# Performance work log

Hardware: AMD Instinct MI355X
Metric: run time of the kernel (lower is better)

The kernel has to match this reference:

```python
import jax, jax.numpy as jnp
import numpy as np

N_NODES = 100000
N_EDGES = 500000
E_HID = 64
IN_DIM = 192  # r_hidden + 2*t_hidden
NEG_SLOPE = 0.01


def setup_inputs() -> dict:
    key = jax.random.key(0)
    ks = jax.random.split(key, 16)
    s_in = 1.0 / np.sqrt(IN_DIM)
    s_e = 1.0 / np.sqrt(E_HID)
    inp = {
        "x_e": jax.random.normal(ks[0], (N_NODES, E_HID), dtype=jnp.float32),
        "x_r": jax.random.normal(ks[1], (N_EDGES, IN_DIM), dtype=jnp.float32),
        "edge_index": jax.random.randint(ks[2], (2, N_EDGES), 0, N_NODES, dtype=jnp.int64),
        "rel_size": jnp.arange(N_EDGES, dtype=jnp.int64),
        "Wr": jax.random.uniform(ks[3], (E_HID, IN_DIM), jnp.float32, -s_in, s_in),
        "br": jax.random.uniform(ks[4], (E_HID,), jnp.float32, -s_in, s_in),
        "Wr1": jax.random.uniform(ks[5], (E_HID, IN_DIM), jnp.float32, -s_in, s_in),
        "br1": jax.random.uniform(ks[6], (E_HID,), jnp.float32, -s_in, s_in),
        "Wr2": jax.random.uniform(ks[7], (E_HID, IN_DIM), jnp.float32, -s_in, s_in),
        "br2": jax.random.uniform(ks[8], (E_HID,), jnp.float32, -s_in, s_in),
        "ah": jax.random.uniform(ks[9], (E_HID,), jnp.float32, -s_e, s_e),
        "ah1": jax.random.uniform(ks[10], (E_HID,), jnp.float32, -s_e, s_e),
        "at": jax.random.uniform(ks[11], (E_HID,), jnp.float32, -s_e, s_e),
        "ar1": jax.random.uniform(ks[12], (E_HID,), jnp.float32, -s_e, s_e),
        "ar2": jax.random.uniform(ks[13], (E_HID,), jnp.float32, -s_e, s_e),
        "ar3": jax.random.uniform(ks[14], (E_HID,), jnp.float32, -s_e, s_e),
    }
    return inp


def _gat_block(x_e, x_r, idx, rel_size, W, b, a_node, a_rel, num_nodes):
    # e_r = w_r(x_r): [E, e_hid]
    e_r = x_r @ W.T + b
    # attention logits per edge: a_node . x_e[idx] + a_rel . e_r
    logits = x_e[idx] @ a_node + e_r @ a_rel  # [E]
    lr = jnp.where(logits > 0, logits, NEG_SLOPE * logits)  # leaky_relu
    # segment softmax over destination segments (idx)
    m = jax.ops.segment_max(lr, idx, num_segments=num_nodes)
    ex = jnp.exp(lr - m[idx])
    s = jax.ops.segment_sum(ex, idx, num_segments=num_nodes)
    alpha = ex / (s[idx] + 1e-16)
    # spmm: out[n] = sum_{e: idx[e]==n} alpha[e] * e_r[rel_size[e]]
    agg = jax.ops.segment_sum(alpha[:, None] * e_r[rel_size], idx, num_segments=num_nodes)
    return x_e + jax.nn.relu(agg)


def reference(x_e, x_r, edge_index, rel_size, Wr, br, Wr1, br1, Wr2, br2,
              ah, ah1, at, ar1, ar2, ar3):
    n = x_e.shape[0]
    h, t = edge_index[0], edge_index[1]
    x_e = _gat_block(x_e, x_r, h, rel_size, Wr, br, ah, ar1, n)
    x_e = _gat_block(x_e, x_r, t, rel_size, Wr1, br1, at, ar2, n)
    x_e = _gat_block(x_e, x_r, h, rel_size, Wr2, br2, ah1, ar3, n)
    return x_e
```

## Files before the change

kernel.cpp:

```cpp
#include <hip/hip_runtime.h>
#include <hip/hip_bf16.h>

typedef __attribute__((ext_vector_type(8))) short short8;
typedef __attribute__((ext_vector_type(4))) float f32x4;

#define DEV __device__ __forceinline__

#define BARRIER() do { asm volatile("s_waitcnt lgkmcnt(0)" ::: "memory"); \
                       __builtin_amdgcn_s_barrier(); \
                       __builtin_amdgcn_sched_barrier(0); } while (0)

DEV unsigned short f2bf(float f) {
    unsigned u = __float_as_uint(f);
    u += 0x7FFFu + ((u >> 16) & 1u);
    return (unsigned short)(u >> 16);
}
DEV float bf2f(unsigned short h) { return __uint_as_float(((unsigned)h) << 16); }
DEV unsigned pk2(float lo, float hi) {
    float2 f; f.x = lo; f.y = hi;
    __hip_bfloat162 h = __float22bfloat162_rn(f);
    unsigned r; __builtin_memcpy(&r, &h, 4);
    return r;
}
union S8 { short8 s; unsigned u[4]; };

__global__ __launch_bounds__(256) void wconv_k(
    const float* __restrict__ W0, const float* __restrict__ W1,
    const float* __restrict__ W2, unsigned short* __restrict__ wbf)
{
    const int i = blockIdx.x * 256 + threadIdx.x;
    if (i >= 3 * 64 * 192) return;
    const int m = i / (64 * 192), r = i % (64 * 192);
    const float* W = (m == 0) ? W0 : ((m == 1) ? W1 : W2);
    wbf[i] = f2bf(W[r]);
}

__global__ __launch_bounds__(256) void gemm_k(
    const float* __restrict__ xr, const unsigned short* __restrict__ wbf,
    const float* __restrict__ b0, const float* __restrict__ b1, const float* __restrict__ b2,
    const float* __restrict__ a0, const float* __restrict__ a1, const float* __restrict__ a2,
    unsigned short* __restrict__ er,
    float* __restrict__ ed0, float* __restrict__ ed1, float* __restrict__ ed2,
    int E, int ntiles, int K)
{
    __shared__ unsigned short As[64 * 192];
    __shared__ float red[12][64];
    const int t = threadIdx.x;
    const int w = t >> 6, l = t & 63, l15 = l & 15, lg = l >> 4;
    const int srow = t >> 2, sq = t & 3;

    short8 bfr[3][6];
#pragma unroll
    for (int i = 0; i < 3; ++i) {
        const int gc = (w * 3 + i) * 16 + l15;
#pragma unroll
        for (int ks = 0; ks < 6; ++ks)
            bfr[i][ks] = *(const short8*)&wbf[(size_t)gc * 192 + ks * 32 + lg * 8];
    }
    float4 biasf[3], arf[3];
#pragma unroll
    for (int i = 0; i < 3; ++i) {
        const int ct = w * 3 + i, m = ct >> 2;
        const int cb_ = ((ct & 3) << 4) + (lg << 2);
        const float* bp = (m == 0) ? b0 : ((m == 1) ? b1 : b2);
        const float* ap = (m == 0) ? a0 : ((m == 1) ? a1 : a2);
        biasf[i] = *(const float4*)(bp + cb_);
        arf[i]  = *(const float4*)(ap + cb_);
    }

    const int G = gridDim.x;
    float4 nv[12];
    if (blockIdx.x < ntiles) {
        const long e = (long)blockIdx.x * 64 + srow;
        const bool ok = e < E;
        const float* sp = xr + e * (long)K + sq * 48;
#pragma unroll
        for (int r = 0; r < 3; ++r)
#pragma unroll
            for (int g2 = 0; g2 < 4; ++g2)
                nv[r * 4 + g2] = ok ? *(const float4*)(sp + r * 16 + g2 * 4)
                                    : make_float4(0.f, 0.f, 0.f, 0.f);
    }

    for (int tile = blockIdx.x; tile < ntiles; tile += G) {
        const long e0 = (long)tile * 64;
        BARRIER();
        {
            const unsigned swz = (unsigned)((srow & 7) << 4);
#pragma unroll
            for (int r = 0; r < 3; ++r) {
                S8 o0, o1;
                o0.u[0] = pk2(nv[r * 4 + 0].x, nv[r * 4 + 0].y);
                o0.u[1] = pk2(nv[r * 4 + 0].z, nv[r * 4 + 0].w);
                o0.u[2] = pk2(nv[r * 4 + 1].x, nv[r * 4 + 1].y);
                o0.u[3] = pk2(nv[r * 4 + 1].z, nv[r * 4 + 1].w);
                o1.u[0] = pk2(nv[r * 4 + 2].x, nv[r * 4 + 2].y);
                o1.u[1] = pk2(nv[r * 4 + 2].z, nv[r * 4 + 2].w);
                o1.u[2] = pk2(nv[r * 4 + 3].x, nv[r * 4 + 3].y);
                o1.u[3] = pk2(nv[r * 4 + 3].z, nv[r * 4 + 3].w);
                const unsigned byte0 = (unsigned)(srow * 384 + (sq * 48 + r * 16) * 2);
                *(short8*)((char*)As + (byte0 ^ swz)) = o0.s;
                *(short8*)((char*)As + ((byte0 + 16) ^ swz)) = o1.s;
            }
        }
        {
            const int nxt = tile + G;
            if (nxt < ntiles) {
                const long e = (long)nxt * 64 + srow;
                const bool ok = e < E;
                const float* sp = xr + e * (long)K + sq * 48;
#pragma unroll
                for (int r = 0; r < 3; ++r)
#pragma unroll
                    for (int g2 = 0; g2 < 4; ++g2)
                        nv[r * 4 + g2] = ok ? *(const float4*)(sp + r * 16 + g2 * 4)
                                            : make_float4(0.f, 0.f, 0.f, 0.f);
            }
        }
        BARRIER();
        f32x4 acc[4][3];
#pragma unroll
        for (int rt = 0; rt < 4; ++rt)
#pragma unroll
            for (int i = 0; i < 3; ++i) acc[rt][i] = (f32x4)(0.f);
#pragma unroll
        for (int ks = 0; ks < 6; ++ks) {
            short8 af[4];
#pragma unroll
            for (int rt = 0; rt < 4; ++rt) {
                const int row = rt * 16 + l15;
                const unsigned byte = (unsigned)(row * 384 + ks * 64 + lg * 16);
                af[rt] = *(const short8*)((const char*)As + (byte ^ ((row & 7) << 4)));
            }
#pragma unroll
            for (int i = 0; i < 3; ++i)
#pragma unroll
                for (int rt = 0; rt < 4; ++rt)
                    acc[rt][i] = __builtin_amdgcn_mfma_f32_16x16x32_bf16(bfr[i][ks], af[rt], acc[rt][i], 0, 0, 0);
        }
#pragma unroll
        for (int i = 0; i < 3; ++i) {
            const int fb = (w * 3 + i) * 16 + (lg << 2);
#pragma unroll
            for (int rt = 0; rt < 4; ++rt) {
                const int edge = rt * 16 + l15;
                const long ee = e0 + edge;
                const float v0 = acc[rt][i][0] + biasf[i].x;
                const float v1 = acc[rt][i][1] + biasf[i].y;
                const float v2 = acc[rt][i][2] + biasf[i].z;
                const float v3 = acc[rt][i][3] + biasf[i].w;
                if (ee < E) {
                    uint2 pkv;
                    pkv.x = pk2(v0, v1);
                    pkv.y = pk2(v2, v3);
                    *(uint2*)(er + (size_t)ee * 192 + fb) = pkv;
                }
                float pd = v0 * arf[i].x + v1 * arf[i].y + v2 * arf[i].z + v3 * arf[i].w;
                pd += __shfl_xor(pd, 16);
                pd += __shfl_xor(pd, 32);
                if (lg == 0) red[w * 3 + i][edge] = pd;
            }
        }
        BARRIER();
        if (t < 64) {
            const long ee = e0 + t;
            if (ee < E) {
                float s0 = 0.f, s1 = 0.f, s2 = 0.f;
#pragma unroll
                for (int q = 0; q < 4; ++q) {
                    s0 += red[q][t]; s1 += red[4 + q][t]; s2 += red[8 + q][t];
                }
                ed0[ee] = s0; ed1[ee] = s1; ed2[ee] = s2;
            }
        }
    }
}

__global__ __launch_bounds__(256) void count2_k(const int* __restrict__ h,
                                                const int* __restrict__ tt,
                                                int* __restrict__ deg, int E, int N)
{
    const int e = blockIdx.x * 256 + threadIdx.x;
    if (e >= E) return;
    atomicAdd(&deg[h[e]], 1);
    atomicAdd(&deg[N + tt[e]], 1);
}

__global__ __launch_bounds__(256) void scan1_k(const int* __restrict__ deg,
                                               int* __restrict__ incl,
                                               int* __restrict__ bsum, int M)
{
    __shared__ int buf[256];
    const int tid = threadIdx.x;
    const int n = blockIdx.x * 256 + tid;
    buf[tid] = (n < M) ? deg[n] : 0;
    __syncthreads();
    for (int d = 1; d < 256; d <<= 1) {
        int v = (tid >= d) ? buf[tid - d] : 0;
        __syncthreads();
        buf[tid] += v;
        __syncthreads();
    }
    if (n < M) incl[n] = buf[tid];
    if (tid == 255) bsum[blockIdx.x] = buf[255];
}

__global__ __launch_bounds__(256) void scan2_k(int* __restrict__ bsum, int nb)
{
    __shared__ int wsum[4];
    const int tid = threadIdx.x, l = tid & 63, wv = tid >> 6;
    int base = 0;
    for (int start = 0; start < nb; start += 1024) {
        const int i0 = start + tid * 4;
        int v0 = 0, v1 = 0, v2 = 0, v3 = 0;
        if (i0 < nb)     v0 = bsum[i0];
        if (i0 + 1 < nb) v1 = bsum[i0 + 1];
        if (i0 + 2 < nb) v2 = bsum[i0 + 2];
        if (i0 + 3 < nb) v3 = bsum[i0 + 3];
        const int tsum = v0 + v1 + v2 + v3;
        int sc = tsum;
#pragma unroll
        for (int d = 1; d < 64; d <<= 1) {
            const int o = __shfl_up(sc, d);
            if (l >= d) sc += o;
        }
        if (l == 63) wsum[wv] = sc;
        __syncthreads();
        int woff = base;
        for (int q = 0; q < wv; ++q) woff += wsum[q];
        int run = woff + sc - tsum;
        run += v0; if (i0 < nb)     bsum[i0] = run;
        run += v1; if (i0 + 1 < nb) bsum[i0 + 1] = run;
        run += v2; if (i0 + 2 < nb) bsum[i0 + 2] = run;
        run += v3; if (i0 + 3 < nb) bsum[i0 + 3] = run;
        base += wsum[0] + wsum[1] + wsum[2] + wsum[3];
        __syncthreads();
    }
}

__global__ __launch_bounds__(256) void off_k(const int* __restrict__ deg,
                                             const int* __restrict__ incl,
                                             const int* __restrict__ bsum,
                                             int* __restrict__ off,
                                             int* __restrict__ cur, int M, int tot)
{
    const int n = blockIdx.x * 256 + threadIdx.x;
    if (n < M) {
        const int prev = (blockIdx.x > 0) ? bsum[blockIdx.x - 1] : 0;
        const int o = prev + incl[n] - deg[n];
        off[n] = o;
        cur[n] = o;
    }
    if (n == 0) off[M] = tot;
}

__global__ __launch_bounds__(256) void fill2_k(const int* __restrict__ h,
                                               const int* __restrict__ tt,
                                               int* __restrict__ cur,
                                               int* __restrict__ elist, int E, int N)
{
    const int e = blockIdx.x * 256 + threadIdx.x;
    if (e >= E) return;
    const int p = atomicAdd(&cur[h[e]], 1);
    elist[p] = e;
    const int p2 = atomicAdd(&cur[N + tt[e]], 1);
    elist[p2] = e;
}

__global__ __launch_bounds__(256, 4) void gat3_k(
    const int* __restrict__ off, const int* __restrict__ elist,
    const float* __restrict__ ed0, const float* __restrict__ ed1,
    const float* __restrict__ ed2, const unsigned short* __restrict__ er,
    const float* __restrict__ xe, float* __restrict__ out,
    const float* __restrict__ an0, const float* __restrict__ an1,
    const float* __restrict__ an2, int N)
{
    __shared__ float sm[4][8][64];
    const int wv = threadIdx.x >> 6;
    const int node = blockIdx.x * 4 + wv;
    if (node >= N) return;
    const int l = threadIdx.x & 63;
    const int g = l >> 3, q = l & 7;

    float x = xe[(size_t)node * 64 + l];

#pragma unroll
    for (int b = 0; b < 3; ++b) {
        const float* edb = (b == 0) ? ed0 : ((b == 1) ? ed1 : ed2);
        const float* anb = (b == 0) ? an0 : ((b == 1) ? an1 : an2);
        const int* offb = off + ((b == 1) ? N : 0);
        const int cb = b * 64;
        const int s0 = offb[node], s1 = offb[node + 1];

        float pv = x * anb[l];
#pragma unroll
        for (int d = 1; d < 64; d <<= 1) pv += __shfl_xor(pv, d);

        float m = -1e30f, s = 0.f;
        f32x4 aA = (f32x4)(0.f), aB = (f32x4)(0.f);
        for (int j = s0; j < s1; j += 8) {
            const int jj = j + g;
            if (jj < s1) {
                const int e = elist[jj];
                const float lg_ = pv + edb[e];
                const float lv = lg_ > 0.f ? lg_ : 0.01f * lg_;
                const short8 v = *(const short8*)(er + (size_t)e * 192 + cb + q * 8);
                const float nm = fmaxf(m, lv);
                const float rs = __expf(m - nm);
                const float wg = __expf(lv - nm);
                s = s * rs + wg;
                aA[0] = aA[0] * rs + wg * bf2f((unsigned short)v[0]);
                aA[1] = aA[1] * rs + wg * bf2f((unsigned short)v[1]);
                aA[2] = aA[2] * rs + wg * bf2f((unsigned short)v[2]);
                aA[3] = aA[3] * rs + wg * bf2f((unsigned short)v[3]);
                aB[0] = aB[0] * rs + wg * bf2f((unsigned short)v[4]);
                aB[1] = aB[1] * rs + wg * bf2f((unsigned short)v[5]);
                aB[2] = aB[2] * rs + wg * bf2f((unsigned short)v[6]);
                aB[3] = aB[3] * rs + wg * bf2f((unsigned short)v[7]);
                m = nm;
            }
        }
        float mt = m;
        mt = fmaxf(mt, __shfl_xor(mt, 8));
        mt = fmaxf(mt, __shfl_xor(mt, 16));
        mt = fmaxf(mt, __shfl_xor(mt, 32));
        const float rs2 = __expf(m - mt);
        s *= rs2;
        s += __shfl_xor(s, 8);
        s += __shfl_xor(s, 16);
        s += __shfl_xor(s, 32);
#pragma unroll
        for (int c = 0; c < 4; ++c) { aA[c] *= rs2; aB[c] *= rs2; }
        *(f32x4*)&sm[wv][g][q * 8] = aA;
        *(f32x4*)&sm[wv][g][q * 8 + 4] = aB;
        asm volatile("s_waitcnt lgkmcnt(0)" ::: "memory");
        __builtin_amdgcn_sched_barrier(0);
        float a = 0.f;
#pragma unroll
        for (int gg = 0; gg < 8; ++gg) a += sm[wv][gg][l];
        asm volatile("s_waitcnt lgkmcnt(0)" ::: "memory");
        __builtin_amdgcn_sched_barrier(0);

        x += fmaxf(a / (s + 1e-16f), 0.f);
    }
    out[(size_t)node * 64 + l] = x;
}

extern "C" void kernel_launch(void* const* d_in, const int* in_sizes, int n_in,
                              void* d_out, int out_size, void* d_ws, size_t ws_size,
                              hipStream_t stream)
{
    const float* xe  = (const float*)d_in[0];
    const float* xr  = (const float*)d_in[1];
    const int*   eix = (const int*)d_in[2];
    const float* Wr  = (const float*)d_in[4];
    const float* br  = (const float*)d_in[5];
    const float* Wr1 = (const float*)d_in[6];
    const float* br1 = (const float*)d_in[7];
    const float* Wr2 = (const float*)d_in[8];
    const float* br2 = (const float*)d_in[9];
    const float* ah  = (const float*)d_in[10];
    const float* ah1 = (const float*)d_in[11];
    const float* at_ = (const float*)d_in[12];
    const float* ar1 = (const float*)d_in[13];
    const float* ar2 = (const float*)d_in[14];
    const float* ar3 = (const float*)d_in[15];

    const int E = in_sizes[3];
    const int N = in_sizes[0] / 64;
    const int K = in_sizes[1] / E;
    const int M = 2 * N;
    float* out = (float*)d_out;

    char* p = (char*)d_ws;
    auto carve = [&](size_t bytes) -> void* {
        void* r = (void*)p;
        p += (bytes + 255) & ~(size_t)255;
        return r;
    };
    const int nb = (M + 255) / 256;
    unsigned short* er = (unsigned short*)carve((size_t)(E + 64) * 192 * 2);
    float* ed0 = (float*)carve((size_t)(E + 64) * 4);
    float* ed1 = (float*)carve((size_t)(E + 64) * 4);
    float* ed2 = (float*)carve((size_t)(E + 64) * 4);
    unsigned short* wbf = (unsigned short*)carve((size_t)3 * 64 * 192 * 2);
    int* off = (int*)carve((size_t)(M + 1) * 4);
    int* elist = (int*)carve((size_t)2 * E * 4);
    int* deg = (int*)carve((size_t)M * 4);
    int* incl = (int*)carve((size_t)M * 4);
    int* cur = (int*)carve((size_t)M * 4);
    int* bsum = (int*)carve((size_t)nb * 4);
    (void)ws_size;

    const int Eg = (E + 255) / 256;
    const int ng = (N + 3) / 4;
    const int ntiles = (E + 63) / 64;
    const int ggrid = ntiles < 1536 ? ntiles : 1536;

    wconv_k<<<(3 * 64 * 192 + 255) / 256, 256, 0, stream>>>(Wr, Wr1, Wr2, wbf);

    hipMemsetAsync(deg, 0, (size_t)M * 4, stream);
    count2_k<<<Eg, 256, 0, stream>>>(eix, eix + E, deg, E, N);
    scan1_k<<<nb, 256, 0, stream>>>(deg, incl, bsum, M);
    scan2_k<<<1, 256, 0, stream>>>(bsum, nb);
    off_k<<<nb, 256, 0, stream>>>(deg, incl, bsum, off, cur, M, 2 * E);
    fill2_k<<<Eg, 256, 0, stream>>>(eix, eix + E, cur, elist, E, N);

    gemm_k<<<ggrid, 256, 0, stream>>>(xr, wbf, br, br1, br2, ar1, ar2, ar3,
                                      er, ed0, ed1, ed2, E, ntiles, K);

    gat3_k<<<ng, 256, 0, stream>>>(off, elist, ed0, ed1, ed2, er, xe, out,
                                   ah, at_, ah1, N);
}
```

Before: 439.4 us.

## Cut GEMM register pressure: drop prefetch, stream weights per k-step, raise occupancy

```diff
diff --git a/kernel.cpp b/kernel.cpp
--- a/kernel.cpp
+++ b/kernel.cpp
@@ -35,7 +35,7 @@
     wbf[i] = f2bf(W[r]);
 }
 
-__global__ __launch_bounds__(256) void gemm_k(
+__global__ __launch_bounds__(256, 4) void gemm_k(
     const float* __restrict__ xr, const unsigned short* __restrict__ wbf,
     const float* __restrict__ b0, const float* __restrict__ b1, const float* __restrict__ b2,
     const float* __restrict__ a0, const float* __restrict__ a1, const float* __restrict__ a2,
@@ -49,74 +49,38 @@
     const int w = t >> 6, l = t & 63, l15 = l & 15, lg = l >> 4;
     const int srow = t >> 2, sq = t & 3;
 
-    short8 bfr[3][6];
-#pragma unroll
-    for (int i = 0; i < 3; ++i) {
-        const int gc = (w * 3 + i) * 16 + l15;
-#pragma unroll
-        for (int ks = 0; ks < 6; ++ks)
-            bfr[i][ks] = *(const short8*)&wbf[(size_t)gc * 192 + ks * 32 + lg * 8];
-    }
-    float4 biasf[3], arf[3];
-#pragma unroll
-    for (int i = 0; i < 3; ++i) {
-        const int ct = w * 3 + i, m = ct >> 2;
-        const int cb_ = ((ct & 3) << 4) + (lg << 2);
-        const float* bp = (m == 0) ? b0 : ((m == 1) ? b1 : b2);
-        const float* ap = (m == 0) ? a0 : ((m == 1) ? a1 : a2);
-        biasf[i] = *(const float4*)(bp + cb_);
-        arf[i]  = *(const float4*)(ap + cb_);
-    }
-
-    const int G = gridDim.x;
-    float4 nv[12];
-    if (blockIdx.x < ntiles) {
-        const long e = (long)blockIdx.x * 64 + srow;
-        const bool ok = e < E;
-        const float* sp = xr + e * (long)K + sq * 48;
-#pragma unroll
-        for (int r = 0; r < 3; ++r)
-#pragma unroll
-            for (int g2 = 0; g2 < 4; ++g2)
-                nv[r * 4 + g2] = ok ? *(const float4*)(sp + r * 16 + g2 * 4)
-                                    : make_float4(0.f, 0.f, 0.f, 0.f);
-    }
-
-    for (int tile = blockIdx.x; tile < ntiles; tile += G) {
+    const unsigned short* wp[3];
+#pragma unroll
+    for (int i = 0; i < 3; ++i)
+        wp[i] = wbf + (size_t)((w * 3 + i) * 16 + l15) * 192 + lg * 8;
+
+    for (int tile = blockIdx.x; tile < ntiles; tile += gridDim.x) {
         const long e0 = (long)tile * 64;
         BARRIER();
         {
+            const long e = e0 + srow;
+            const bool ok = e < E;
+            const float* sp = xr + e * (long)K + sq * 48;
             const unsigned swz = (unsigned)((srow & 7) << 4);
 #pragma unroll
             for (int r = 0; r < 3; ++r) {
+                float4 v0 = make_float4(0.f, 0.f, 0.f, 0.f), v1 = v0, v2 = v0, v3 = v0;
+                if (ok) {
+                    v0 = *(const float4*)(sp + r * 16);
+                    v1 = *(const float4*)(sp + r * 16 + 4);
+                    v2 = *(const float4*)(sp + r * 16 + 8);
+                    v3 = *(const float4*)(sp + r * 16 + 12);
+                }
                 S8 o0, o1;
-                o0.u[0] = pk2(nv[r * 4 + 0].x, nv[r * 4 + 0].y);
-                o0.u[1] = pk2(nv[r * 4 + 0].z, nv[r * 4 + 0].w);
-                o0.u[2] = pk2(nv[r * 4 + 1].x, nv[r * 4 + 1].y);
-                o0.u[3] = pk2(nv[r * 4 + 1].z, nv[r * 4 + 1].w);
-                o1.u[0] = pk2(nv[r * 4 + 2].x, nv[r * 4 + 2].y);
-                o1.u[1] = pk2(nv[r * 4 + 2].z, nv[r * 4 + 2].w);
-                o1.u[2] = pk2(nv[r * 4 + 3].x, nv[r * 4 + 3].y);
-                o1.u[3] = pk2(nv[r * 4 + 3].z, nv[r * 4 + 3].w);
+                o0.u[0] = pk2(v0.x, v0.y); o0.u[1] = pk2(v0.z, v0.w);
+                o0.u[2] = pk2(v1.x, v1.y); o0.u[3] = pk2(v1.z, v1.w);
+                o1.u[0] = pk2(v2.x, v2.y); o1.u[1] = pk2(v2.z, v2.w);
+                o1.u[2] = pk2(v3.x, v3.y); o1.u[3] = pk2(v3.z, v3.w);
                 const unsigned byte0 = (unsigned)(srow * 384 + (sq * 48 + r * 16) * 2);
                 *(short8*)((char*)As + (byte0 ^ swz)) = o0.s;
                 *(short8*)((char*)As + ((byte0 + 16) ^ swz)) = o1.s;
             }
         }
-        {
-            const int nxt = tile + G;
-            if (nxt < ntiles) {
-                const long e = (long)nxt * 64 + srow;
-                const bool ok = e < E;
-                const float* sp = xr + e * (long)K + sq * 48;
-#pragma unroll
-                for (int r = 0; r < 3; ++r)
-#pragma unroll
-                    for (int g2 = 0; g2 < 4; ++g2)
-                        nv[r * 4 + g2] = ok ? *(const float4*)(sp + r * 16 + g2 * 4)
-                                            : make_float4(0.f, 0.f, 0.f, 0.f);
-            }
-        }
         BARRIER();
         f32x4 acc[4][3];
 #pragma unroll
@@ -125,6 +89,10 @@
             for (int i = 0; i < 3; ++i) acc[rt][i] = (f32x4)(0.f);
 #pragma unroll
         for (int ks = 0; ks < 6; ++ks) {
+            short8 bq[3];
+#pragma unroll
+            for (int i = 0; i < 3; ++i)
+                bq[i] = *(const short8*)(wp[i] + ks * 32);
             short8 af[4];
 #pragma unroll
             for (int rt = 0; rt < 4; ++rt) {
@@ -136,29 +104,35 @@
             for (int i = 0; i < 3; ++i)
 #pragma unroll
                 for (int rt = 0; rt < 4; ++rt)
-                    acc[rt][i] = __builtin_amdgcn_mfma_f32_16x16x32_bf16(bfr[i][ks], af[rt], acc[rt][i], 0, 0, 0);
+                    acc[rt][i] = __builtin_amdgcn_mfma_f32_16x16x32_bf16(bq[i], af[rt], acc[rt][i], 0, 0, 0);
         }
 #pragma unroll
         for (int i = 0; i < 3; ++i) {
-            const int fb = (w * 3 + i) * 16 + (lg << 2);
+            const int ct = w * 3 + i, m = ct >> 2;
+            const int cb_ = ((ct & 3) << 4) + (lg << 2);
+            const float* bp = (m == 0) ? b0 : ((m == 1) ? b1 : b2);
+            const float* ap = (m == 0) ? a0 : ((m == 1) ? a1 : a2);
+            const float4 bb = *(const float4*)(bp + cb_);
+            const float4 aa = *(const float4*)(ap + cb_);
+            const int fb = ct * 16 + (lg << 2);
 #pragma unroll
             for (int rt = 0; rt < 4; ++rt) {
                 const int edge = rt * 16 + l15;
                 const long ee = e0 + edge;
-                const float v0 = acc[rt][i][0] + biasf[i].x;
-                const float v1 = acc[rt][i][1] + biasf[i].y;
-                const float v2 = acc[rt][i][2] + biasf[i].z;
-                const float v3 = acc[rt][i][3] + biasf[i].w;
+                const float v0 = acc[rt][i][0] + bb.x;
+                const float v1 = acc[rt][i][1] + bb.y;
+                const float v2 = acc[rt][i][2] + bb.z;
+                const float v3 = acc[rt][i][3] + bb.w;
                 if (ee < E) {
                     uint2 pkv;
                     pkv.x = pk2(v0, v1);
                     pkv.y = pk2(v2, v3);
                     *(uint2*)(er + (size_t)ee * 192 + fb) = pkv;
                 }
-                float pd = v0 * arf[i].x + v1 * arf[i].y + v2 * arf[i].z + v3 * arf[i].w;
+                float pd = v0 * aa.x + v1 * aa.y + v2 * aa.z + v3 * aa.w;
                 pd += __shfl_xor(pd, 16);
                 pd += __shfl_xor(pd, 32);
-                if (lg == 0) red[w * 3 + i][edge] = pd;
+                if (lg == 0) red[ct][edge] = pd;
             }
         }
         BARRIER();
@@ -267,7 +241,7 @@
     elist[p2] = e;
 }
 
-__global__ __launch_bounds__(256, 4) void gat3_k(
+__global__ __launch_bounds__(256, 6) void gat3_k(
     const int* __restrict__ off, const int* __restrict__ elist,
     const float* __restrict__ ed0, const float* __restrict__ ed1,
     const float* __restrict__ ed2, const unsigned short* __restrict__ er,
@@ -395,7 +369,7 @@
     const int Eg = (E + 255) / 256;
     const int ng = (N + 3) / 4;
     const int ntiles = (E + 63) / 64;
-    const int ggrid = ntiles < 1536 ? ntiles : 1536;
+    const int ggrid = ntiles < 2048 ? ntiles : 2048;
 
     wconv_k<<<(3 * 64 * 192 + 255) / 256, 256, 0, stream>>>(Wr, Wr1, Wr2, wbf);
 
```

Measured after the change: 467.8 us. 6.5% more time.
